# Kernel tuning notes

Hardware: AMD Instinct MI355X
Metric: run time of the kernel (lower is better)

## Reference

```python
import jax, jax.numpy as jnp
import numpy as np

D_MODEL = 1024
HEADS = 16
D_HEAD = D_MODEL // HEADS


def setup_inputs() -> dict:
    key = jax.random.key(0)
    ks = jax.random.split(key, 7)
    s = 1.0 / np.sqrt(D_MODEL)
    x = jax.random.normal(ks[0], (4, 2048, D_MODEL), dtype=jnp.float32)
    Wq = jax.random.uniform(ks[1], (D_MODEL, D_MODEL), jnp.float32, -s, s)
    bq = jax.random.uniform(ks[2], (D_MODEL,), jnp.float32, -s, s)
    Wk = jax.random.uniform(ks[3], (D_MODEL, D_MODEL), jnp.float32, -s, s)
    bk = jax.random.uniform(ks[4], (D_MODEL,), jnp.float32, -s, s)
    Wv = jax.random.uniform(ks[5], (D_MODEL, D_MODEL), jnp.float32, -s, s)
    bv = jax.random.uniform(ks[6], (D_MODEL,), jnp.float32, -s, s)
    return {"x": x, "Wq": Wq, "bq": bq, "Wk": Wk, "bk": bk, "Wv": Wv, "bv": bv}


def reference(x, Wq, bq, Wk, bk, Wv, bv):
    B, S, D = x.shape
    # QKV projections, split heads: [B, H, S, Dh]
    def split(t):
        return t.reshape(B, S, HEADS, D_HEAD).transpose(0, 2, 1, 3)
    q = split(x @ Wq + bq)
    k = split(x @ Wk + bk)
    v = split(x @ Wv + bv)
    scores = jnp.einsum('bhqd,bhkd->bhqk', q, k) / np.sqrt(D_HEAD).astype(jnp.float32)
    attn = jax.nn.softmax(scores, axis=-1)
    out = jnp.einsum('bhqk,bhkd->bhqd', attn, v)
    return out.transpose(0, 2, 1, 3).reshape(B, S, D)
```

## Files before the change

### kernel.cpp

```cpp
#include <hip/hip_runtime.h>

typedef _Float16 f16;
typedef __attribute__((ext_vector_type(2))) _Float16 f16x2;
typedef __attribute__((ext_vector_type(2))) __fp16   hf16x2;
typedef __attribute__((ext_vector_type(4))) _Float16 f16x4;
typedef __attribute__((ext_vector_type(8))) _Float16 f16x8;
typedef __attribute__((ext_vector_type(4))) float    f32x4;

#define D_MODEL 1024
#define HEADS   16
#define DH      64
#define SEQ     2048
#define BATCH   4
#define SSCALE  0.1803368801111204f

__device__ __forceinline__ void gload_lds16(const void* g, void* lds) {
  __builtin_amdgcn_global_load_lds(
      (const __attribute__((address_space(1))) unsigned int*)g,
      (__attribute__((address_space(3))) unsigned int*)lds, 16, 0, 0);
}

__global__ __launch_bounds__(256) void cast_x_kernel(const float* __restrict__ x,
                                                     f16* __restrict__ xb) {
  int i = blockIdx.x * 256 + threadIdx.x;
  float4 v = ((const float4*)x)[i];
  f16x4 h;
  h[0] = (f16)v.x; h[1] = (f16)v.y; h[2] = (f16)v.z; h[3] = (f16)v.w;
  ((f16x4*)xb)[i] = h;
}

__global__ __launch_bounds__(256) void wtrans_kernel(const float* __restrict__ Wq,
                                                     const float* __restrict__ Wk,
                                                     const float* __restrict__ Wv,
                                                     f16* __restrict__ wt) {
  const float* W = blockIdx.z == 0 ? Wq : (blockIdx.z == 1 ? Wk : Wv);
  f16* out = wt + (size_t)blockIdx.z * D_MODEL * D_MODEL;
  __shared__ float tile[64][65];
  int n0 = blockIdx.x * 64, k0 = blockIdx.y * 64;
  int tx = threadIdx.x & 63, ty = threadIdx.x >> 6;
#pragma unroll
  for (int r = 0; r < 16; ++r)
    tile[ty * 16 + r][tx] = W[(size_t)(k0 + ty * 16 + r) * D_MODEL + n0 + tx];
  __syncthreads();
#pragma unroll
  for (int r = 0; r < 16; ++r)
    out[(size_t)(n0 + ty * 16 + r) * D_MODEL + k0 + tx] = (f16)tile[tx][ty * 16 + r];
}

__global__ __launch_bounds__(256) void qkv_gemm_kernel(
    const f16* __restrict__ xb, const f16* __restrict__ wt_all,
    const float* __restrict__ bq, const float* __restrict__ bk, const float* __restrict__ bv,
    f16* __restrict__ qout, f16* __restrict__ kout, f16* __restrict__ vtout) {
  const int z = blockIdx.z;
  const f16* wt = wt_all + (size_t)z * D_MODEL * D_MODEL;
  const float* bias = z == 0 ? bq : (z == 1 ? bk : bv);
  const int n0 = blockIdx.x * 128, m0 = blockIdx.y * 128;

  __shared__ f16 As[128 * 64];
  __shared__ f16 Bs[128 * 64];

  const int tid = threadIdx.x;
  const int lane = tid & 63, w = tid >> 6;
  const int quad = lane >> 4, l15 = lane & 15;
  const int wm = w & 1, wn = w >> 1;

  int aoff[2], boff[2];
#pragma unroll
  for (int ks = 0; ks < 2; ++ks) {
    int pc = ((ks * 4 + quad) ^ (l15 & 7)) * 8;
    aoff[ks] = wm * 4096 + l15 * 64 + pc;
    boff[ks] = wn * 4096 + l15 * 64 + pc;
  }

  f32x4 acc[4][4];
#pragma unroll
  for (int i = 0; i < 4; ++i)
#pragma unroll
    for (int j = 0; j < 4; ++j) acc[i][j] = (f32x4){0.f, 0.f, 0.f, 0.f};

  for (int k0 = 0; k0 < D_MODEL; k0 += 64) {
#pragma unroll
    for (int c = 0; c < 4; ++c) {
      int slot = (w * 4 + c) * 64 + lane;
      int row = slot >> 3, col = slot & 7;
      int cl = col ^ (row & 7);
      gload_lds16(xb + (size_t)(m0 + row) * D_MODEL + k0 + cl * 8, As + (w * 4 + c) * 512);
      gload_lds16(wt + (size_t)(n0 + row) * D_MODEL + k0 + cl * 8, Bs + (w * 4 + c) * 512);
    }
    __syncthreads();
#pragma unroll
    for (int ks = 0; ks < 2; ++ks) {
      f16x8 a[4], b[4];
#pragma unroll
      for (int mt = 0; mt < 4; ++mt) a[mt] = *(const f16x8*)(As + aoff[ks] + mt * 1024);
#pragma unroll
      for (int nt = 0; nt < 4; ++nt) b[nt] = *(const f16x8*)(Bs + boff[ks] + nt * 1024);
#pragma unroll
      for (int mt = 0; mt < 4; ++mt)
#pragma unroll
        for (int nt = 0; nt < 4; ++nt)
          acc[mt][nt] = __builtin_amdgcn_mfma_f32_16x16x32_f16(a[mt], b[nt], acc[mt][nt], 0, 0, 0);
    }
    __syncthreads();
  }

  const float sc = (z == 0) ? SSCALE : 1.0f;
  float bcol[4];
#pragma unroll
  for (int nt = 0; nt < 4; ++nt) bcol[nt] = bias[n0 + wn * 64 + nt * 16 + l15];

  if (z < 2) {
    f16* out = (z == 0) ? qout : kout;
#pragma unroll
    for (int mt = 0; mt < 4; ++mt) {
      int mbase = m0 + wm * 64 + mt * 16 + quad * 4;
#pragma unroll
      for (int nt = 0; nt < 4; ++nt) {
        int n = n0 + wn * 64 + nt * 16 + l15;
        int h = n >> 6, dh = n & 63;
#pragma unroll
        for (int r = 0; r < 4; ++r) {
          int m = mbase + r;
          int b = m >> 11, s = m & 2047;
          out[((size_t)(b * HEADS + h) * SEQ + s) * DH + dh] = (f16)((acc[mt][nt][r] + bcol[nt]) * sc);
        }
      }
    }
  } else {
#pragma unroll
    for (int mt = 0; mt < 4; ++mt) {
      int mbase = m0 + wm * 64 + mt * 16 + quad * 4;
      int b = mbase >> 11, s = mbase & 2047;
#pragma unroll
      for (int nt = 0; nt < 4; ++nt) {
        int n = n0 + wn * 64 + nt * 16 + l15;
        int h = n >> 6, dh = n & 63;
        f16x4 v;
#pragma unroll
        for (int r = 0; r < 4; ++r) v[r] = (f16)(acc[mt][nt][r] + bcol[nt]);
        *(f16x4*)(vtout + ((size_t)(b * HEADS + h) * DH + dh) * SEQ + s) = v;
      }
    }
  }
}

__global__ __launch_bounds__(256) void attn_kernel(
    const f16* __restrict__ q, const f16* __restrict__ k, const f16* __restrict__ vt,
    float* __restrict__ out) {
  const int bh = blockIdx.x;
  const int s0 = blockIdx.y * 128;
  const int b = bh >> 4, h = bh & 15;
  const int tid = threadIdx.x, lane = tid & 63, w = tid >> 6;
  const int quad = lane >> 4, l15 = lane & 15;
  const int qh = quad >> 1, q1 = quad & 1;

  __shared__ f16 Ks[128 * 64];
  __shared__ f16 Vs[64 * 128];

  const f16* qbase = q + ((size_t)bh * SEQ + s0 + w * 32) * DH;
  const f16* kbase = k + (size_t)bh * SEQ * DH;
  const f16* vbase = vt + (size_t)bh * DH * SEQ;

  f16x8 qf[2][2];
#pragma unroll
  for (int qt = 0; qt < 2; ++qt)
#pragma unroll
    for (int ks = 0; ks < 2; ++ks)
      qf[qt][ks] = *(const f16x8*)(qbase + (qt * 16 + l15) * DH + ks * 32 + quad * 8);

  int koff[2];
  koff[0] = l15 * 64 + ((quad ^ (l15 & 7)) * 8);
  koff[1] = l15 * 64 + (((4 + quad) ^ (l15 & 7)) * 8);
  int voff[8];
#pragma unroll
  for (int ks = 0; ks < 8; ++ks)
    voff[ks] = l15 * 128 + (((ks * 2 + qh) ^ l15) * 8) + q1 * 4;

  float lsum[2] = {0.f, 0.f};
  f32x4 o[4][2];
#pragma unroll
  for (int i = 0; i < 4; ++i)
#pragma unroll
    for (int j = 0; j < 2; ++j) o[i][j] = (f32x4){0.f, 0.f, 0.f, 0.f};

  for (int kt = 0; kt < SEQ / 128; ++kt) {
#pragma unroll
    for (int c = 0; c < 4; ++c) {
      int slot = (w * 4 + c) * 64 + lane;
      int row = slot >> 3, col = slot & 7;
      int cl = col ^ (row & 7);
      gload_lds16(kbase + (size_t)(kt * 128 + row) * DH + cl * 8, Ks + (w * 4 + c) * 512);
      int vrow = slot >> 4, vcol = slot & 15;
      int vcl = vcol ^ (vrow & 15);
      gload_lds16(vbase + (size_t)vrow * SEQ + kt * 128 + vcl * 8, Vs + (w * 4 + c) * 512);
    }
    __syncthreads();

    f32x4 st[8][2];
#pragma unroll
    for (int mt = 0; mt < 8; ++mt)
#pragma unroll
      for (int qt = 0; qt < 2; ++qt) st[mt][qt] = (f32x4){0.f, 0.f, 0.f, 0.f};
#pragma unroll
    for (int mt = 0; mt < 8; ++mt)
#pragma unroll
      for (int ks = 0; ks < 2; ++ks) {
        f16x8 af = *(const f16x8*)(Ks + koff[ks] + mt * 1024);
#pragma unroll
        for (int qt = 0; qt < 2; ++qt)
          st[mt][qt] = __builtin_amdgcn_mfma_f32_16x16x32_f16(af, qf[qt][ks], st[mt][qt], 0, 0, 0);
      }

#pragma unroll
    for (int ks = 0; ks < 8; ++ks) {
      f16x4 pb[2];
#pragma unroll
      for (int qt = 0; qt < 2; ++qt) {
        float e0 = __builtin_amdgcn_exp2f(st[ks][qt][0]);
        float e1 = __builtin_amdgcn_exp2f(st[ks][qt][1]);
        float e2 = __builtin_amdgcn_exp2f(st[ks][qt][2]);
        float e3 = __builtin_amdgcn_exp2f(st[ks][qt][3]);
        lsum[qt] += (e0 + e1) + (e2 + e3);
        hf16x2 h01 = __builtin_amdgcn_cvt_pkrtz(e0, e1);
        hf16x2 h23 = __builtin_amdgcn_cvt_pkrtz(e2, e3);
        f16x2 p01 = __builtin_bit_cast(f16x2, h01);
        f16x2 p23 = __builtin_bit_cast(f16x2, h23);
        pb[qt][0] = p01[0]; pb[qt][1] = p01[1]; pb[qt][2] = p23[0]; pb[qt][3] = p23[1];
      }
#pragma unroll
      for (int mt = 0; mt < 4; ++mt) {
        f16x4 va = *(const f16x4*)(Vs + voff[ks] + mt * 2048);
#pragma unroll
        for (int qt = 0; qt < 2; ++qt)
          o[mt][qt] = __builtin_amdgcn_mfma_f32_16x16x16f16(va, pb[qt], o[mt][qt], 0, 0, 0);
      }
    }
    __syncthreads();
  }

#pragma unroll
  for (int qt = 0; qt < 2; ++qt) {
    float l = lsum[qt];
    l += __shfl_xor(l, 16, 64);
    l += __shfl_xor(l, 32, 64);
    float inv = 1.f / l;
    int sq = s0 + w * 32 + qt * 16 + l15;
    float* obase = out + ((size_t)b * SEQ + sq) * D_MODEL + h * DH;
#pragma unroll
    for (int mt = 0; mt < 4; ++mt) {
      f32x4 vv;
#pragma unroll
      for (int r = 0; r < 4; ++r) vv[r] = o[mt][qt][r] * inv;
      *(f32x4*)(obase + mt * 16 + quad * 4) = vv;
    }
  }
}

extern "C" void kernel_launch(void* const* d_in, const int* in_sizes, int n_in,
                              void* d_out, int out_size, void* d_ws, size_t ws_size,
                              hipStream_t stream) {
  const float* x  = (const float*)d_in[0];
  const float* Wq = (const float*)d_in[1];
  const float* bq = (const float*)d_in[2];
  const float* Wk = (const float*)d_in[3];
  const float* bk = (const float*)d_in[4];
  const float* Wv = (const float*)d_in[5];
  const float* bv = (const float*)d_in[6];
  float* out = (float*)d_out;

  char* ws = (char*)d_ws;
  f16* xb = (f16*)ws;
  f16* wt = (f16*)(ws + (size_t)16 * 1024 * 1024);
  f16* q  = (f16*)(ws + (size_t)22 * 1024 * 1024);
  f16* kk = q + (size_t)BATCH * SEQ * D_MODEL;
  f16* vt = kk + (size_t)BATCH * SEQ * D_MODEL;

  cast_x_kernel<<<8192, 256, 0, stream>>>(x, xb);
  wtrans_kernel<<<dim3(16, 16, 3), 256, 0, stream>>>(Wq, Wk, Wv, wt);
  qkv_gemm_kernel<<<dim3(8, 64, 3), 256, 0, stream>>>(xb, wt, bq, bk, bv, q, kk, vt);
  attn_kernel<<<dim3(64, 16), 256, 0, stream>>>(q, kk, vt, out);
}
```

Baseline: 273.0 us.

## Double-buffer LDS in QKV GEMM and attention, enlarge GEMM tile to 256x256

The QKV GEMM moves to 256x256 tiles with 512 threads and a K-step of 32. Its A/B tiles are double-buffered in LDS, so the global loads for the next step are issued before the MFMAs on the current buffer and one barrier per iteration is dropped. The attention kernel likewise double-buffers 64-key K/V tiles and prefetches the next tile while computing. Occupancy hints are added to launch_bounds. This costs more accumulator registers per thread and relies on a single barrier to separate the prefetch writes from reads of the other buffer.

After: 289.3 us. 6.0% more time.

```diff
diff --git a/kernel.cpp b/kernel.cpp
--- a/kernel.cpp
+++ b/kernel.cpp
@@ -47,61 +47,66 @@
     out[(size_t)(n0 + ty * 16 + r) * D_MODEL + k0 + tx] = (f16)tile[tx][ty * 16 + r];
 }
 
-__global__ __launch_bounds__(256) void qkv_gemm_kernel(
+__global__ __launch_bounds__(512, 2) void qkv_gemm_kernel(
     const f16* __restrict__ xb, const f16* __restrict__ wt_all,
     const float* __restrict__ bq, const float* __restrict__ bk, const float* __restrict__ bv,
     f16* __restrict__ qout, f16* __restrict__ kout, f16* __restrict__ vtout) {
   const int z = blockIdx.z;
   const f16* wt = wt_all + (size_t)z * D_MODEL * D_MODEL;
   const float* bias = z == 0 ? bq : (z == 1 ? bk : bv);
-  const int n0 = blockIdx.x * 128, m0 = blockIdx.y * 128;
-
-  __shared__ f16 As[128 * 64];
-  __shared__ f16 Bs[128 * 64];
+  const int n0 = blockIdx.x * 256, m0 = blockIdx.y * 256;
+
+  __shared__ f16 As[2][256 * 32];
+  __shared__ f16 Bs[2][256 * 32];
 
   const int tid = threadIdx.x;
   const int lane = tid & 63, w = tid >> 6;
   const int quad = lane >> 4, l15 = lane & 15;
   const int wm = w & 1, wn = w >> 1;
 
-  int aoff[2], boff[2];
-#pragma unroll
-  for (int ks = 0; ks < 2; ++ks) {
-    int pc = ((ks * 4 + quad) ^ (l15 & 7)) * 8;
-    aoff[ks] = wm * 4096 + l15 * 64 + pc;
-    boff[ks] = wn * 4096 + l15 * 64 + pc;
-  }
-
-  f32x4 acc[4][4];
-#pragma unroll
-  for (int i = 0; i < 4; ++i)
+  const int pce = (quad ^ (l15 & 3)) * 8;
+  const int aoff = wm * 4096 + l15 * 32 + pce;
+  const int boff = wn * 2048 + l15 * 32 + pce;
+
+  int srow[2], scl[2];
+#pragma unroll
+  for (int c = 0; c < 2; ++c) {
+    int slot = (w * 2 + c) * 64 + lane;
+    srow[c] = slot >> 2;
+    scl[c] = (slot & 3) ^ (srow[c] & 3);
+  }
+
+  f32x4 acc[8][4];
+#pragma unroll
+  for (int i = 0; i < 8; ++i)
 #pragma unroll
     for (int j = 0; j < 4; ++j) acc[i][j] = (f32x4){0.f, 0.f, 0.f, 0.f};
 
-  for (int k0 = 0; k0 < D_MODEL; k0 += 64) {
-#pragma unroll
-    for (int c = 0; c < 4; ++c) {
-      int slot = (w * 4 + c) * 64 + lane;
-      int row = slot >> 3, col = slot & 7;
-      int cl = col ^ (row & 7);
-      gload_lds16(xb + (size_t)(m0 + row) * D_MODEL + k0 + cl * 8, As + (w * 4 + c) * 512);
-      gload_lds16(wt + (size_t)(n0 + row) * D_MODEL + k0 + cl * 8, Bs + (w * 4 + c) * 512);
-    }
+#pragma unroll
+  for (int c = 0; c < 2; ++c) {
+    gload_lds16(xb + (size_t)(m0 + srow[c]) * D_MODEL + scl[c] * 8, &As[0][(w * 2 + c) * 512]);
+    gload_lds16(wt + (size_t)(n0 + srow[c]) * D_MODEL + scl[c] * 8, &Bs[0][(w * 2 + c) * 512]);
+  }
+
+  for (int k0 = 0; k0 < D_MODEL; k0 += 32) {
+    const int buf = (k0 >> 5) & 1;
+    const int kn = (k0 + 32) & (D_MODEL - 1);
     __syncthreads();
 #pragma unroll
-    for (int ks = 0; ks < 2; ++ks) {
-      f16x8 a[4], b[4];
-#pragma unroll
-      for (int mt = 0; mt < 4; ++mt) a[mt] = *(const f16x8*)(As + aoff[ks] + mt * 1024);
-#pragma unroll
-      for (int nt = 0; nt < 4; ++nt) b[nt] = *(const f16x8*)(Bs + boff[ks] + nt * 1024);
-#pragma unroll
-      for (int mt = 0; mt < 4; ++mt)
-#pragma unroll
-        for (int nt = 0; nt < 4; ++nt)
-          acc[mt][nt] = __builtin_amdgcn_mfma_f32_16x16x32_f16(a[mt], b[nt], acc[mt][nt], 0, 0, 0);
-    }
-    __syncthreads();
+    for (int c = 0; c < 2; ++c) {
+      gload_lds16(xb + (size_t)(m0 + srow[c]) * D_MODEL + kn + scl[c] * 8, &As[buf ^ 1][(w * 2 + c) * 512]);
+      gload_lds16(wt + (size_t)(n0 + srow[c]) * D_MODEL + kn + scl[c] * 8, &Bs[buf ^ 1][(w * 2 + c) * 512]);
+    }
+    f16x8 a[8], b[4];
+#pragma unroll
+    for (int mt = 0; mt < 8; ++mt) a[mt] = *(const f16x8*)(&As[buf][aoff + mt * 512]);
+#pragma unroll
+    for (int nt = 0; nt < 4; ++nt) b[nt] = *(const f16x8*)(&Bs[buf][boff + nt * 512]);
+#pragma unroll
+    for (int mt = 0; mt < 8; ++mt)
+#pragma unroll
+      for (int nt = 0; nt < 4; ++nt)
+        acc[mt][nt] = __builtin_amdgcn_mfma_f32_16x16x32_f16(a[mt], b[nt], acc[mt][nt], 0, 0, 0);
   }
 
   const float sc = (z == 0) ? SSCALE : 1.0f;
@@ -112,8 +117,8 @@
   if (z < 2) {
     f16* out = (z == 0) ? qout : kout;
 #pragma unroll
-    for (int mt = 0; mt < 4; ++mt) {
-      int mbase = m0 + wm * 64 + mt * 16 + quad * 4;
+    for (int mt = 0; mt < 8; ++mt) {
+      int mbase = m0 + wm * 128 + mt * 16 + quad * 4;
 #pragma unroll
       for (int nt = 0; nt < 4; ++nt) {
         int n = n0 + wn * 64 + nt * 16 + l15;
@@ -128,8 +133,8 @@
     }
   } else {
 #pragma unroll
-    for (int mt = 0; mt < 4; ++mt) {
-      int mbase = m0 + wm * 64 + mt * 16 + quad * 4;
+    for (int mt = 0; mt < 8; ++mt) {
+      int mbase = m0 + wm * 128 + mt * 16 + quad * 4;
       int b = mbase >> 11, s = mbase & 2047;
 #pragma unroll
       for (int nt = 0; nt < 4; ++nt) {
@@ -144,7 +149,7 @@
   }
 }
 
-__global__ __launch_bounds__(256) void attn_kernel(
+__global__ __launch_bounds__(256, 4) void attn_kernel(
     const f16* __restrict__ q, const f16* __restrict__ k, const f16* __restrict__ vt,
     float* __restrict__ out) {
   const int bh = blockIdx.x;
@@ -154,8 +159,8 @@
   const int quad = lane >> 4, l15 = lane & 15;
   const int qh = quad >> 1, q1 = quad & 1;
 
-  __shared__ f16 Ks[128 * 64];
-  __shared__ f16 Vs[64 * 128];
+  __shared__ f16 Ks[2][64 * 64];
+  __shared__ f16 Vs[2][64 * 64];
 
   const f16* qbase = q + ((size_t)bh * SEQ + s0 + w * 32) * DH;
   const f16* kbase = k + (size_t)bh * SEQ * DH;
@@ -171,10 +176,18 @@
   int koff[2];
   koff[0] = l15 * 64 + ((quad ^ (l15 & 7)) * 8);
   koff[1] = l15 * 64 + (((4 + quad) ^ (l15 & 7)) * 8);
-  int voff[8];
-#pragma unroll
-  for (int ks = 0; ks < 8; ++ks)
-    voff[ks] = l15 * 128 + (((ks * 2 + qh) ^ l15) * 8) + q1 * 4;
+  int voff[4];
+#pragma unroll
+  for (int ks = 0; ks < 4; ++ks)
+    voff[ks] = l15 * 64 + (((ks * 2 + qh) ^ (l15 & 7)) * 8) + q1 * 4;
+
+  int srow[2], scl[2];
+#pragma unroll
+  for (int c = 0; c < 2; ++c) {
+    int slot = (w * 2 + c) * 64 + lane;
+    srow[c] = slot >> 3;
+    scl[c] = (slot & 7) ^ (srow[c] & 7);
+  }
 
   float lsum[2] = {0.f, 0.f};
   f32x4 o[4][2];
@@ -183,36 +196,39 @@
 #pragma unroll
     for (int j = 0; j < 2; ++j) o[i][j] = (f32x4){0.f, 0.f, 0.f, 0.f};
 
-  for (int kt = 0; kt < SEQ / 128; ++kt) {
-#pragma unroll
-    for (int c = 0; c < 4; ++c) {
-      int slot = (w * 4 + c) * 64 + lane;
-      int row = slot >> 3, col = slot & 7;
-      int cl = col ^ (row & 7);
-      gload_lds16(kbase + (size_t)(kt * 128 + row) * DH + cl * 8, Ks + (w * 4 + c) * 512);
-      int vrow = slot >> 4, vcol = slot & 15;
-      int vcl = vcol ^ (vrow & 15);
-      gload_lds16(vbase + (size_t)vrow * SEQ + kt * 128 + vcl * 8, Vs + (w * 4 + c) * 512);
-    }
+#pragma unroll
+  for (int c = 0; c < 2; ++c) {
+    gload_lds16(kbase + (size_t)srow[c] * DH + scl[c] * 8, &Ks[0][(w * 2 + c) * 512]);
+    gload_lds16(vbase + (size_t)srow[c] * SEQ + scl[c] * 8, &Vs[0][(w * 2 + c) * 512]);
+  }
+
+  for (int kt = 0; kt < SEQ / 64; ++kt) {
+    const int buf = kt & 1;
+    const int ktn = (kt + 1) & (SEQ / 64 - 1);
     __syncthreads();
-
-    f32x4 st[8][2];
-#pragma unroll
-    for (int mt = 0; mt < 8; ++mt)
+#pragma unroll
+    for (int c = 0; c < 2; ++c) {
+      gload_lds16(kbase + (size_t)(ktn * 64 + srow[c]) * DH + scl[c] * 8, &Ks[buf ^ 1][(w * 2 + c) * 512]);
+      gload_lds16(vbase + (size_t)srow[c] * SEQ + ktn * 64 + scl[c] * 8, &Vs[buf ^ 1][(w * 2 + c) * 512]);
+    }
+
+    f32x4 st[4][2];
+#pragma unroll
+    for (int mt = 0; mt < 4; ++mt)
 #pragma unroll
       for (int qt = 0; qt < 2; ++qt) st[mt][qt] = (f32x4){0.f, 0.f, 0.f, 0.f};
 #pragma unroll
-    for (int mt = 0; mt < 8; ++mt)
+    for (int mt = 0; mt < 4; ++mt)
 #pragma unroll
       for (int ks = 0; ks < 2; ++ks) {
-        f16x8 af = *(const f16x8*)(Ks + koff[ks] + mt * 1024);
+        f16x8 af = *(const f16x8*)(&Ks[buf][koff[ks] + mt * 1024]);
 #pragma unroll
         for (int qt = 0; qt < 2; ++qt)
           st[mt][qt] = __builtin_amdgcn_mfma_f32_16x16x32_f16(af, qf[qt][ks], st[mt][qt], 0, 0, 0);
       }
 
 #pragma unroll
-    for (int ks = 0; ks < 8; ++ks) {
+    for (int ks = 0; ks < 4; ++ks) {
       f16x4 pb[2];
 #pragma unroll
       for (int qt = 0; qt < 2; ++qt) {
@@ -229,13 +245,12 @@
       }
 #pragma unroll
       for (int mt = 0; mt < 4; ++mt) {
-        f16x4 va = *(const f16x4*)(Vs + voff[ks] + mt * 2048);
+        f16x4 va = *(const f16x4*)(&Vs[buf][voff[ks] + mt * 1024]);
 #pragma unroll
         for (int qt = 0; qt < 2; ++qt)
           o[mt][qt] = __builtin_amdgcn_mfma_f32_16x16x16f16(va, pb[qt], o[mt][qt], 0, 0, 0);
       }
     }
-    __syncthreads();
   }
 
 #pragma unroll
@@ -277,6 +292,6 @@
 
   cast_x_kernel<<<8192, 256, 0, stream>>>(x, xb);
   wtrans_kernel<<<dim3(16, 16, 3), 256, 0, stream>>>(Wq, Wk, Wv, wt);
-  qkv_gemm_kernel<<<dim3(8, 64, 3), 256, 0, stream>>>(xb, wt, bq, bk, bv, q, kk, vt);
+  qkv_gemm_kernel<<<dim3(4, 32, 3), 512, 0, stream>>>(xb, wt, bq, bk, bv, q, kk, vt);
   attn_kernel<<<dim3(64, 16), 256, 0, stream>>>(q, kk, vt, out);
 }
```
